# Kernel optimization log

Hardware: AMD Instinct MI355X
Metric: run time of the kernel (lower is better)

## Reference

```python
import jax, jax.numpy as jnp
import numpy as np

H = 1024  # hidden size

def _gru_layer(x, h0_l, w_ih_l, w_hh_l, b_ih_l, b_hh_l):
    # x: [T,B,I]; precompute input gates for all timesteps (like addmm in the kernel)
    x_gates = jnp.einsum('tbi,gi->tbg', x, w_ih_l) + b_ih_l  # [T,B,3H]

    def step(h, xg):
        # h: [B,H]; xg: [B,3H]
        h_gates = h @ w_hh_l.T + b_hh_l  # [B,3H]
        xr, xz, xn = xg[:, :H], xg[:, H:2*H], xg[:, 2*H:]
        hr, hz, hn = h_gates[:, :H], h_gates[:, H:2*H], h_gates[:, 2*H:]
        r = jax.nn.sigmoid(xr + hr)
        z = jax.nn.sigmoid(xz + hz)
        n = jnp.tanh(xn + r * hn)
        h_new = (1.0 - z) * n + z * h
        return h_new, h_new

    h_final, seq_out = jax.lax.scan(step, h0_l, x_gates)
    return h_final, seq_out


def setup_inputs() -> dict:
    key = jax.random.key(0)
    ks = jax.random.split(key, 6)
    T, B, I, L = 512, 64, 1024, 2
    s = 1.0 / np.sqrt(H)
    return {
        'x': jax.random.normal(ks[0], (T, B, I), dtype=jnp.float32),
        'h0': jax.random.normal(ks[1], (L, B, H), dtype=jnp.float32),
        'w_ih': jax.random.normal(ks[2], (L, 3 * H, I), dtype=jnp.float32) * s,
        'w_hh': jax.random.normal(ks[3], (L, 3 * H, H), dtype=jnp.float32) * s,
        'b_ih': jax.random.normal(ks[4], (L, 3 * H), dtype=jnp.float32) * s,
        'b_hh': jax.random.normal(ks[5], (L, 3 * H), dtype=jnp.float32) * s,
    }


def reference(x, h0, w_ih, w_hh, b_ih, b_hh):
    num_layers = h0.shape[0]
    h_n = []
    cur = x
    for l in range(num_layers):
        h_final, seq_out = _gru_layer(cur, h0[l], w_ih[l], w_hh[l], b_ih[l], b_hh[l])
        h_n.append(h_final)
        cur = seq_out  # layer output becomes next layer's input
    # kernel returns only the final hidden state of every layer, in fp32
    return jnp.stack(h_n, axis=0)  # [L,B,H]
```

## Files before the change

### kernel.cpp

```cpp
#include <hip/hip_runtime.h>

typedef unsigned short u16;
typedef unsigned long long u64;
typedef __attribute__((ext_vector_type(8))) short short8;
typedef __attribute__((ext_vector_type(4))) float f32x4;

#define HH 1024
#define BB 64
#define TT 512
#define G3 3072
#define NBLK 192
#define NS 513
#define SLOT (BB * HH)
#define FSTRIDE 32
#define RING 32

__device__ __forceinline__ u16 f2b(float f) {
  unsigned u = __float_as_uint(f);
  unsigned r = (u + 0x7fffu + ((u >> 16) & 1u)) >> 16;
  return (u16)r;
}
__device__ __forceinline__ float b2f(u16 h) {
  return __uint_as_float(((unsigned)h) << 16);
}
__device__ __forceinline__ float ftanh(float x) {
  x = fminf(15.f, fmaxf(-15.f, x));
  float e = __expf(2.f * x);
  return (e - 1.f) / (e + 1.f);
}

__device__ __forceinline__ void st_u32_agent(unsigned* p, unsigned v) {
  __hip_atomic_store(p, v, __ATOMIC_RELAXED, __HIP_MEMORY_SCOPE_AGENT);
}
__device__ __forceinline__ unsigned ld_u32_agent(const unsigned* p) {
  return __hip_atomic_load(p, __ATOMIC_RELAXED, __HIP_MEMORY_SCOPE_AGENT);
}


__global__ void f32_to_bf16_k(const float* __restrict__ s, u16* __restrict__ d, int n) {
  int stride = gridDim.x * blockDim.x * 4;
  for (int i = (blockIdx.x * blockDim.x + threadIdx.x) * 4; i < n; i += stride) {
    float4 v = *(const float4*)(s + i);
    uint2 p;
    p.x = (unsigned)f2b(v.x) | ((unsigned)f2b(v.y) << 16);
    p.y = (unsigned)f2b(v.z) | ((unsigned)f2b(v.w) << 16);
    *(uint2*)(d + i) = p;
  }
}

__global__ void init_h_k(const float* __restrict__ h0in, u16* __restrict__ hbuf0,
                         u16* __restrict__ hbuf1) {
  int i = blockIdx.x * blockDim.x + threadIdx.x;
  if (i < BB * HH) {
    hbuf0[i] = f2b(h0in[i]);
    hbuf1[i] = f2b(h0in[BB * HH + i]);
  }
}


__global__ __launch_bounds__(256) void gemm_xg_k(
    const u16* __restrict__ A, const u16* __restrict__ Wt,
    const float* __restrict__ bias, u16* __restrict__ C) {
  const int bm = blockIdx.x / 24;
  const int bn = blockIdx.x % 24;
  const int m0 = bm * 128, n0 = bn * 128;
  __shared__ __align__(16) u16 al[128 * 40];
  __shared__ __align__(16) u16 bl[128 * 40];
  const int tid = threadIdx.x;
  const int w = tid >> 6, l = tid & 63;
  const int wr = w >> 1, wc = w & 1;
  const int c0 = tid, c1 = tid + 256;
  const int r0 = c0 >> 2, s0 = c0 & 3, r1 = c1 >> 2, s1 = c1 & 3;

  const f32x4 fzero = {0.f, 0.f, 0.f, 0.f};
  f32x4 acc[4][4];
#pragma unroll
  for (int i = 0; i < 4; ++i)
#pragma unroll
    for (int j = 0; j < 4; ++j) acc[i][j] = fzero;

  const u16* a0p = A + (size_t)(m0 + r0) * 1024 + s0 * 8;
  const u16* a1p = A + (size_t)(m0 + r1) * 1024 + s1 * 8;
  const u16* b0p = Wt + (size_t)(n0 + r0) * 1024 + s0 * 8;
  const u16* b1p = Wt + (size_t)(n0 + r1) * 1024 + s1 * 8;

  int4 va0 = *(const int4*)(a0p);
  int4 va1 = *(const int4*)(a1p);
  int4 vb0 = *(const int4*)(b0p);
  int4 vb1 = *(const int4*)(b1p);

  for (int kt = 0; kt < 32; ++kt) {
    __syncthreads();
    *(int4*)&al[r0 * 40 + s0 * 8] = va0;
    *(int4*)&al[r1 * 40 + s1 * 8] = va1;
    *(int4*)&bl[r0 * 40 + s0 * 8] = vb0;
    *(int4*)&bl[r1 * 40 + s1 * 8] = vb1;
    __syncthreads();
    if (kt < 31) {
      va0 = *(const int4*)(a0p + (kt + 1) * 32);
      va1 = *(const int4*)(a1p + (kt + 1) * 32);
      vb0 = *(const int4*)(b0p + (kt + 1) * 32);
      vb1 = *(const int4*)(b1p + (kt + 1) * 32);
    }
    short8 af[4], bf[4];
#pragma unroll
    for (int i = 0; i < 4; ++i)
      af[i] = *(const short8*)&al[(wr * 64 + i * 16 + (l & 15)) * 40 + (l >> 4) * 8];
#pragma unroll
    for (int j = 0; j < 4; ++j)
      bf[j] = *(const short8*)&bl[(wc * 64 + j * 16 + (l & 15)) * 40 + (l >> 4) * 8];
#pragma unroll
    for (int i = 0; i < 4; ++i)
#pragma unroll
      for (int j = 0; j < 4; ++j)
        acc[i][j] = __builtin_amdgcn_mfma_f32_16x16x32_bf16(af[i], bf[j], acc[i][j], 0, 0, 0);
  }

#pragma unroll
  for (int i = 0; i < 4; ++i) {
#pragma unroll
    for (int j = 0; j < 4; ++j) {
      int col = n0 + wc * 64 + j * 16 + (l & 15);
      float bv = bias[col];
#pragma unroll
      for (int q = 0; q < 4; ++q) {
        int row = m0 + wr * 64 + i * 16 + (l >> 4) * 4 + q;
        C[(size_t)row * G3 + col] = f2b(acc[i][j][q] + bv);
      }
    }
  }
}


__global__ __launch_bounds__(256, 1) void gru_scan13_k(
    const u16* __restrict__ xg0,
    const u16* __restrict__ whh0, const u16* __restrict__ wih1,
    const u16* __restrict__ whh1,
    const float* __restrict__ bhh0, const float* __restrict__ bih1,
    const float* __restrict__ bhh1,
    const float* __restrict__ h0in,
    u16* __restrict__ hbuf0, u16* __restrict__ hbuf1,
    u16* __restrict__ xg1ring, float* __restrict__ out,
    unsigned* __restrict__ flags0, unsigned* __restrict__ flags1,
    unsigned* __restrict__ flags2) {
  const int blk = blockIdx.x;
  const int grp = blk >> 6;
  const int sub = blk & 63;
  const int tid = threadIdx.x;
  const int w = tid >> 6, l = tid & 63;
  const int lrow = l & 15;
  const int kb = (l >> 4) * 8;
  const int myrow0 = w * 16 + (l >> 4) * 4;
  const size_t arow = (size_t)(w * 16 + lrow) * HH + kb;
  const f32x4 fzero = {0.f, 0.f, 0.f, 0.f};

  __shared__ __align__(16) u16 wlds[48 * 1024];
  {
    const u16* Wsrc = (grp == 0) ? whh0 : (grp == 1) ? wih1 : whh1;
    for (int i = tid; i < 6144; i += 256) {
      int r = i >> 7;
      int c = i & 127;
      int g = r >> 4;
      int wrow = g * HH + sub * 16 + (r & 15);
      int4 v = *(const int4*)(Wsrc + (size_t)wrow * 1024 + c * 8);
      int idx = r * 1024 + ((c * 8) ^ ((r & 7) << 3));
      *(int4*)&wlds[idx] = v;
    }
  }
  __syncthreads();
  __builtin_amdgcn_fence(__ATOMIC_ACQUIRE, "agent");

  const int j = sub * 16 + lrow;
  const int sx = (lrow & 7) << 3;
  const int myf = (sub * 4 + w) * FSTRIDE;
  const int plf = (l * 4 + w) * FSTRIDE;

  if (grp == 0) {
    const float bhr = bhh0[j], bhz = bhh0[HH + j], bhn = bhh0[2 * HH + j];
    float hreg[4];
#pragma unroll
    for (int q = 0; q < 4; ++q) hreg[q] = h0in[(myrow0 + q) * HH + j];

    for (int t = 0; t < TT; ++t) {
      u16 xrv[4], xzv[4], xnv[4];
      const u16* xp = xg0 + (size_t)t * BB * G3;
#pragma unroll
      for (int q = 0; q < 4; ++q) {
        const u16* rp = xp + (size_t)(myrow0 + q) * G3;
        xrv[q] = rp[j]; xzv[q] = rp[HH + j]; xnv[q] = rp[2 * HH + j];
      }
      if (t > 0) {
        for (;;) {
          unsigned a0 = ld_u32_agent(&flags0[plf]);
          if (__all(a0 >= (unsigned)t)) break;
        }
      }
      __builtin_amdgcn_fence(__ATOMIC_ACQUIRE, "workgroup");

      const u16* Ap = hbuf0 + (size_t)t * SLOT + arow;
      short8 ar[32];
#pragma unroll
      for (int ks = 0; ks < 32; ++ks) ar[ks] = *(const short8*)(Ap + ks * 32);

      f32x4 acc0 = fzero, acc1 = fzero, acc2 = fzero;
#pragma unroll
      for (int ks = 0; ks < 32; ++ks) {
        int ke = kb + ks * 32;
        short8 b0 = *(const short8*)&wlds[(lrow) * 1024 + (ke ^ sx)];
        short8 b1 = *(const short8*)&wlds[(16 + lrow) * 1024 + (ke ^ sx)];
        short8 b2 = *(const short8*)&wlds[(32 + lrow) * 1024 + (ke ^ sx)];
        acc0 = __builtin_amdgcn_mfma_f32_16x16x32_bf16(ar[ks], b0, acc0, 0, 0, 0);
        acc1 = __builtin_amdgcn_mfma_f32_16x16x32_bf16(ar[ks], b1, acc1, 0, 0, 0);
        acc2 = __builtin_amdgcn_mfma_f32_16x16x32_bf16(ar[ks], b2, acc2, 0, 0, 0);
      }

      u16* hbn = hbuf0 + (size_t)(t + 1) * SLOT;
#pragma unroll
      for (int q = 0; q < 4; ++q) {
        float rr = acc0[q] + bhr + b2f(xrv[q]);
        float zz = acc1[q] + bhz + b2f(xzv[q]);
        float nn = acc2[q] + bhn;
        float r = 1.f / (1.f + __expf(-rr));
        float z = 1.f / (1.f + __expf(-zz));
        float n = ftanh(b2f(xnv[q]) + r * nn);
        float hv = (1.f - z) * n + z * hreg[q];
        hreg[q] = hv;
        int hb = (int)f2b(hv);
        int nb = __shfl_xor(hb, 1);
        if ((l & 1) == 0) {
          unsigned pk = (unsigned)(u16)hb | (((unsigned)(u16)nb) << 16);
          st_u32_agent((unsigned*)(hbn + (size_t)(myrow0 + q) * HH + j), pk);
        }
      }
      asm volatile("s_waitcnt vmcnt(0)" ::: "memory");
      if (l == 0) st_u32_agent(&flags0[myf], (unsigned)(t + 1));
    }
#pragma unroll
    for (int q = 0; q < 4; ++q) out[(size_t)(myrow0 + q) * HH + j] = hreg[q];

  } else if (grp == 1) {
    const float bir = bih1[j], biz = bih1[HH + j], bin = bih1[2 * HH + j];

    for (int t = 1; t <= TT; ++t) {
      for (;;) {
        unsigned a0 = ld_u32_agent(&flags0[plf]);
        unsigned f2 = ld_u32_agent(&flags2[myf]);
        int ok = (a0 >= (unsigned)t) && ((int)f2 >= t - RING);
        if (__all(ok)) break;
      }
      __builtin_amdgcn_fence(__ATOMIC_ACQUIRE, "workgroup");

      const u16* Ap = hbuf0 + (size_t)t * SLOT + arow;
      short8 ar[32];
#pragma unroll
      for (int ks = 0; ks < 32; ++ks) ar[ks] = *(const short8*)(Ap + ks * 32);

      f32x4 acc0 = fzero, acc1 = fzero, acc2 = fzero;
#pragma unroll
      for (int ks = 0; ks < 32; ++ks) {
        int ke = kb + ks * 32;
        short8 b0 = *(const short8*)&wlds[(lrow) * 1024 + (ke ^ sx)];
        short8 b1 = *(const short8*)&wlds[(16 + lrow) * 1024 + (ke ^ sx)];
        short8 b2 = *(const short8*)&wlds[(32 + lrow) * 1024 + (ke ^ sx)];
        acc0 = __builtin_amdgcn_mfma_f32_16x16x32_bf16(ar[ks], b0, acc0, 0, 0, 0);
        acc1 = __builtin_amdgcn_mfma_f32_16x16x32_bf16(ar[ks], b1, acc1, 0, 0, 0);
        acc2 = __builtin_amdgcn_mfma_f32_16x16x32_bf16(ar[ks], b2, acc2, 0, 0, 0);
      }

      u16* ox = xg1ring + (size_t)(t & (RING - 1)) * (BB * G3);
#pragma unroll
      for (int q = 0; q < 4; ++q) {
        int row = myrow0 + q;
        int a0v = (int)f2b(acc0[q] + bir); int a0n = __shfl_xor(a0v, 1);
        int a1v = (int)f2b(acc1[q] + biz); int a1n = __shfl_xor(a1v, 1);
        int a2v = (int)f2b(acc2[q] + bin); int a2n = __shfl_xor(a2v, 1);
        if ((l & 1) == 0) {
          st_u32_agent((unsigned*)(ox + (size_t)row * G3 + j),
                       (unsigned)(u16)a0v | (((unsigned)(u16)a0n) << 16));
          st_u32_agent((unsigned*)(ox + (size_t)row * G3 + HH + j),
                       (unsigned)(u16)a1v | (((unsigned)(u16)a1n) << 16));
          st_u32_agent((unsigned*)(ox + (size_t)row * G3 + 2 * HH + j),
                       (unsigned)(u16)a2v | (((unsigned)(u16)a2n) << 16));
        }
      }
      asm volatile("s_waitcnt vmcnt(0)" ::: "memory");
      if (l == 0) st_u32_agent(&flags1[myf], (unsigned)t);
    }

  } else {
    const float bhr = bhh1[j], bhz = bhh1[HH + j], bhn = bhh1[2 * HH + j];
    float hreg[4];
#pragma unroll
    for (int q = 0; q < 4; ++q) hreg[q] = h0in[BB * HH + (myrow0 + q) * HH + j];
    const int jpair = j & ~1;
    const int sel = (j & 1) * 16;

    for (int t = 1; t <= TT; ++t) {
      for (;;) {
        unsigned f1 = ld_u32_agent(&flags1[myf]);
        unsigned a2 = ld_u32_agent(&flags2[plf]);
        int ok = (f1 >= (unsigned)t) && (a2 >= (unsigned)(t - 1));
        if (__all(ok)) break;
      }
      __builtin_amdgcn_fence(__ATOMIC_ACQUIRE, "workgroup");

      const u16* ox = xg1ring + (size_t)(t & (RING - 1)) * (BB * G3);
      unsigned pr[4], pz[4], pn[4];
#pragma unroll
      for (int q = 0; q < 4; ++q) {
        const u16* rp = ox + (size_t)(myrow0 + q) * G3;
        pr[q] = ld_u32_agent((const unsigned*)(rp + jpair));
        pz[q] = ld_u32_agent((const unsigned*)(rp + HH + jpair));
        pn[q] = ld_u32_agent((const unsigned*)(rp + 2 * HH + jpair));
      }
      const u16* Ap = hbuf1 + (size_t)(t - 1) * SLOT + arow;
      short8 ar[32];
#pragma unroll
      for (int ks = 0; ks < 32; ++ks) ar[ks] = *(const short8*)(Ap + ks * 32);

      f32x4 acc0 = fzero, acc1 = fzero, acc2 = fzero;
#pragma unroll
      for (int ks = 0; ks < 32; ++ks) {
        int ke = kb + ks * 32;
        short8 b0 = *(const short8*)&wlds[(lrow) * 1024 + (ke ^ sx)];
        short8 b1 = *(const short8*)&wlds[(16 + lrow) * 1024 + (ke ^ sx)];
        short8 b2 = *(const short8*)&wlds[(32 + lrow) * 1024 + (ke ^ sx)];
        acc0 = __builtin_amdgcn_mfma_f32_16x16x32_bf16(ar[ks], b0, acc0, 0, 0, 0);
        acc1 = __builtin_amdgcn_mfma_f32_16x16x32_bf16(ar[ks], b1, acc1, 0, 0, 0);
        acc2 = __builtin_amdgcn_mfma_f32_16x16x32_bf16(ar[ks], b2, acc2, 0, 0, 0);
      }

      u16* hbn = hbuf1 + (size_t)t * SLOT;
#pragma unroll
      for (int q = 0; q < 4; ++q) {
        float rr = acc0[q] + bhr + b2f((u16)(pr[q] >> sel));
        float zz = acc1[q] + bhz + b2f((u16)(pz[q] >> sel));
        float nn = acc2[q] + bhn;
        float r = 1.f / (1.f + __expf(-rr));
        float z = 1.f / (1.f + __expf(-zz));
        float n = ftanh(b2f((u16)(pn[q] >> sel)) + r * nn);
        float hv = (1.f - z) * n + z * hreg[q];
        hreg[q] = hv;
        int hb = (int)f2b(hv);
        int nb = __shfl_xor(hb, 1);
        if ((l & 1) == 0) {
          unsigned pk = (unsigned)(u16)hb | (((unsigned)(u16)nb) << 16);
          st_u32_agent((unsigned*)(hbn + (size_t)(myrow0 + q) * HH + j), pk);
        }
      }
      asm volatile("s_waitcnt vmcnt(0)" ::: "memory");
      if (l == 0) st_u32_agent(&flags2[myf], (unsigned)t);
    }
#pragma unroll
    for (int q = 0; q < 4; ++q) out[BB * HH + (size_t)(myrow0 + q) * HH + j] = hreg[q];
  }
}


extern "C" void kernel_launch(void* const* d_in, const int* in_sizes, int n_in,
                              void* d_out, int out_size, void* d_ws, size_t ws_size,
                              hipStream_t stream) {
  const float* x   = (const float*)d_in[0];
  const float* h0  = (const float*)d_in[1];
  const float* wih = (const float*)d_in[2];
  const float* whh = (const float*)d_in[3];
  const float* bih = (const float*)d_in[4];
  const float* bhh = (const float*)d_in[5];
  float* out = (float*)d_out;

  char* ws = (char*)d_ws;
  size_t off = 0;
  auto alloc = [&](size_t bytes) -> void* {
    void* p = ws + off;
    off += (bytes + 255) & ~(size_t)255;
    return p;
  };
  u16* xg0   = (u16*)alloc((size_t)TT * BB * G3 * 2);
  u16* wihb  = (u16*)alloc((size_t)2 * G3 * HH * 2);
  u16* whhb  = (u16*)alloc((size_t)2 * G3 * HH * 2);
  size_t hbytes = (size_t)2 * NS * SLOT * 2;
  size_t xbytes = (size_t)TT * BB * HH * 2;
  char* un = (char*)alloc(hbytes > xbytes ? hbytes : xbytes);
  u16* xbf   = (u16*)un;
  u16* hbuf0 = (u16*)un;
  u16* hbuf1 = hbuf0 + (size_t)NS * SLOT;
  u16* xg1ring = (u16*)alloc((size_t)RING * BB * G3 * 2);
  unsigned* flags0 = (unsigned*)alloc(256 * FSTRIDE * 4);
  unsigned* flags1 = (unsigned*)alloc(256 * FSTRIDE * 4);
  unsigned* flags2 = (unsigned*)alloc(256 * FSTRIDE * 4);

  hipMemsetAsync(flags0, 0, 256 * FSTRIDE * 4, stream);
  hipMemsetAsync(flags1, 0, 256 * FSTRIDE * 4, stream);
  hipMemsetAsync(flags2, 0, 256 * FSTRIDE * 4, stream);
  f32_to_bf16_k<<<2048, 256, 0, stream>>>(x, xbf, TT * BB * HH);
  f32_to_bf16_k<<<512, 256, 0, stream>>>(wih, wihb, 2 * G3 * HH);
  f32_to_bf16_k<<<512, 256, 0, stream>>>(whh, whhb, 2 * G3 * HH);

  gemm_xg_k<<<6144, 256, 0, stream>>>(xbf, wihb, bih, xg0);

  init_h_k<<<256, 256, 0, stream>>>(h0, hbuf0, hbuf1);

  gru_scan13_k<<<NBLK, 256, 0, stream>>>(xg0,
                                         whhb, wihb + (size_t)G3 * HH, whhb + (size_t)G3 * HH,
                                         bhh, bih + G3, bhh + G3, h0,
                                         hbuf0, hbuf1, xg1ring, out,
                                         flags0, flags1, flags2);
}
```

Before: 5.391 ms.

## Stream recurrent GEMM over K chunks as producer blocks signal readiness

Replaces the all-or-nothing spin-wait before each step's recurrent GEMM with a single ballot over per-block ready flags. Each K chunk of the MFMA loop waits only for the two producer blocks that own those hidden columns, so compute can start while slower producers finish. Flags are coarsened from one per wave to one per block, published by thread 0 after a __syncthreads and a release fence. In exchange, the A-operand loads are no longer batched ahead of the MFMA loop and are issued inside a loop with data-dependent polling, which may expose global-load latency.

```diff
diff --git a/kernel.cpp b/kernel.cpp
--- a/kernel.cpp
+++ b/kernel.cpp
@@ -132,7 +132,30 @@
 }
 
 
-__global__ __launch_bounds__(256, 1) void gru_scan13_k(
+#define INORDER_GEMM(FLAGS, TGT, AP)                                          \
+  {                                                                           \
+    unsigned fv = ld_u32_agent(&FLAGS[l * FSTRIDE]);                          \
+    u64 ready = __ballot(fv >= (unsigned)(TGT));                              \
+    __builtin_amdgcn_fence(__ATOMIC_ACQUIRE, "workgroup");                    \
+    _Pragma("unroll")                                                         \
+    for (int ks = 0; ks < 32; ++ks) {                                         \
+      while (((ready >> (2 * ks)) & 3ull) != 3ull) {                          \
+        fv = ld_u32_agent(&FLAGS[l * FSTRIDE]);                               \
+        ready = __ballot(fv >= (unsigned)(TGT));                              \
+        __builtin_amdgcn_fence(__ATOMIC_ACQUIRE, "workgroup");                \
+      }                                                                       \
+      short8 a = *(const short8*)((AP) + ks * 32);                            \
+      int ke = kb + ks * 32;                                                  \
+      short8 b0 = *(const short8*)&wlds[(lrow) * 1024 + (ke ^ sx)];           \
+      short8 b1 = *(const short8*)&wlds[(16 + lrow) * 1024 + (ke ^ sx)];      \
+      short8 b2 = *(const short8*)&wlds[(32 + lrow) * 1024 + (ke ^ sx)];      \
+      acc0 = __builtin_amdgcn_mfma_f32_16x16x32_bf16(a, b0, acc0, 0, 0, 0);   \
+      acc1 = __builtin_amdgcn_mfma_f32_16x16x32_bf16(a, b1, acc1, 0, 0, 0);   \
+      acc2 = __builtin_amdgcn_mfma_f32_16x16x32_bf16(a, b2, acc2, 0, 0, 0);   \
+    }                                                                         \
+  }
+
+__global__ __launch_bounds__(256, 1) void gru_scan15_k(
     const u16* __restrict__ xg0,
     const u16* __restrict__ whh0, const u16* __restrict__ wih1,
     const u16* __restrict__ whh1,
@@ -172,8 +195,6 @@
 
   const int j = sub * 16 + lrow;
   const int sx = (lrow & 7) << 3;
-  const int myf = (sub * 4 + w) * FSTRIDE;
-  const int plf = (l * 4 + w) * FSTRIDE;
 
   if (grp == 0) {
     const float bhr = bhh0[j], bhz = bhh0[HH + j], bhn = bhh0[2 * HH + j];
@@ -189,29 +210,23 @@
         const u16* rp = xp + (size_t)(myrow0 + q) * G3;
         xrv[q] = rp[j]; xzv[q] = rp[HH + j]; xnv[q] = rp[2 * HH + j];
       }
-      if (t > 0) {
-        for (;;) {
-          unsigned a0 = ld_u32_agent(&flags0[plf]);
-          if (__all(a0 >= (unsigned)t)) break;
+
+      const u16* Ap = hbuf0 + (size_t)t * SLOT + arow;
+      f32x4 acc0 = fzero, acc1 = fzero, acc2 = fzero;
+      if (t == 0) {
+#pragma unroll
+        for (int ks = 0; ks < 32; ++ks) {
+          short8 a = *(const short8*)(Ap + ks * 32);
+          int ke = kb + ks * 32;
+          short8 b0 = *(const short8*)&wlds[(lrow) * 1024 + (ke ^ sx)];
+          short8 b1 = *(const short8*)&wlds[(16 + lrow) * 1024 + (ke ^ sx)];
+          short8 b2 = *(const short8*)&wlds[(32 + lrow) * 1024 + (ke ^ sx)];
+          acc0 = __builtin_amdgcn_mfma_f32_16x16x32_bf16(a, b0, acc0, 0, 0, 0);
+          acc1 = __builtin_amdgcn_mfma_f32_16x16x32_bf16(a, b1, acc1, 0, 0, 0);
+          acc2 = __builtin_amdgcn_mfma_f32_16x16x32_bf16(a, b2, acc2, 0, 0, 0);
         }
-      }
-      __builtin_amdgcn_fence(__ATOMIC_ACQUIRE, "workgroup");
-
-      const u16* Ap = hbuf0 + (size_t)t * SLOT + arow;
-      short8 ar[32];
-#pragma unroll
-      for (int ks = 0; ks < 32; ++ks) ar[ks] = *(const short8*)(Ap + ks * 32);
-
-      f32x4 acc0 = fzero, acc1 = fzero, acc2 = fzero;
-#pragma unroll
-      for (int ks = 0; ks < 32; ++ks) {
-        int ke = kb + ks * 32;
-        short8 b0 = *(const short8*)&wlds[(lrow) * 1024 + (ke ^ sx)];
-        short8 b1 = *(const short8*)&wlds[(16 + lrow) * 1024 + (ke ^ sx)];
-        short8 b2 = *(const short8*)&wlds[(32 + lrow) * 1024 + (ke ^ sx)];
-        acc0 = __builtin_amdgcn_mfma_f32_16x16x32_bf16(ar[ks], b0, acc0, 0, 0, 0);
-        acc1 = __builtin_amdgcn_mfma_f32_16x16x32_bf16(ar[ks], b1, acc1, 0, 0, 0);
-        acc2 = __builtin_amdgcn_mfma_f32_16x16x32_bf16(ar[ks], b2, acc2, 0, 0, 0);
+      } else {
+        INORDER_GEMM(flags0, t, Ap)
       }
 
       u16* hbn = hbuf0 + (size_t)(t + 1) * SLOT;
@@ -232,8 +247,12 @@
           st_u32_agent((unsigned*)(hbn + (size_t)(myrow0 + q) * HH + j), pk);
         }
       }
-      asm volatile("s_waitcnt vmcnt(0)" ::: "memory");
-      if (l == 0) st_u32_agent(&flags0[myf], (unsigned)(t + 1));
+
+      __syncthreads();
+      if (tid == 0) {
+        __builtin_amdgcn_fence(__ATOMIC_RELEASE, "workgroup");
+        st_u32_agent(&flags0[sub * FSTRIDE], (unsigned)(t + 1));
+      }
     }
 #pragma unroll
     for (int q = 0; q < 4; ++q) out[(size_t)(myrow0 + q) * HH + j] = hreg[q];
@@ -243,29 +262,13 @@
 
     for (int t = 1; t <= TT; ++t) {
       for (;;) {
-        unsigned a0 = ld_u32_agent(&flags0[plf]);
-        unsigned f2 = ld_u32_agent(&flags2[myf]);
-        int ok = (a0 >= (unsigned)t) && ((int)f2 >= t - RING);
-        if (__all(ok)) break;
-      }
-      __builtin_amdgcn_fence(__ATOMIC_ACQUIRE, "workgroup");
+        unsigned f2 = ld_u32_agent(&flags2[sub * FSTRIDE]);
+        if ((int)f2 >= t - RING) break;
+      }
 
       const u16* Ap = hbuf0 + (size_t)t * SLOT + arow;
-      short8 ar[32];
-#pragma unroll
-      for (int ks = 0; ks < 32; ++ks) ar[ks] = *(const short8*)(Ap + ks * 32);
-
       f32x4 acc0 = fzero, acc1 = fzero, acc2 = fzero;
-#pragma unroll
-      for (int ks = 0; ks < 32; ++ks) {
-        int ke = kb + ks * 32;
-        short8 b0 = *(const short8*)&wlds[(lrow) * 1024 + (ke ^ sx)];
-        short8 b1 = *(const short8*)&wlds[(16 + lrow) * 1024 + (ke ^ sx)];
-        short8 b2 = *(const short8*)&wlds[(32 + lrow) * 1024 + (ke ^ sx)];
-        acc0 = __builtin_amdgcn_mfma_f32_16x16x32_bf16(ar[ks], b0, acc0, 0, 0, 0);
-        acc1 = __builtin_amdgcn_mfma_f32_16x16x32_bf16(ar[ks], b1, acc1, 0, 0, 0);
-        acc2 = __builtin_amdgcn_mfma_f32_16x16x32_bf16(ar[ks], b2, acc2, 0, 0, 0);
-      }
+      INORDER_GEMM(flags0, t, Ap)
 
       u16* ox = xg1ring + (size_t)(t & (RING - 1)) * (BB * G3);
 #pragma unroll
@@ -283,8 +286,12 @@
                        (unsigned)(u16)a2v | (((unsigned)(u16)a2n) << 16));
         }
       }
-      asm volatile("s_waitcnt vmcnt(0)" ::: "memory");
-      if (l == 0) st_u32_agent(&flags1[myf], (unsigned)t);
+
+      __syncthreads();
+      if (tid == 0) {
+        __builtin_amdgcn_fence(__ATOMIC_RELEASE, "workgroup");
+        st_u32_agent(&flags1[sub * FSTRIDE], (unsigned)t);
+      }
     }
 
   } else {
@@ -297,10 +304,8 @@
 
     for (int t = 1; t <= TT; ++t) {
       for (;;) {
-        unsigned f1 = ld_u32_agent(&flags1[myf]);
-        unsigned a2 = ld_u32_agent(&flags2[plf]);
-        int ok = (f1 >= (unsigned)t) && (a2 >= (unsigned)(t - 1));
-        if (__all(ok)) break;
+        unsigned f1 = ld_u32_agent(&flags1[sub * FSTRIDE]);
+        if (f1 >= (unsigned)t) break;
       }
       __builtin_amdgcn_fence(__ATOMIC_ACQUIRE, "workgroup");
 
@@ -313,22 +318,10 @@
         pz[q] = ld_u32_agent((const unsigned*)(rp + HH + jpair));
         pn[q] = ld_u32_agent((const unsigned*)(rp + 2 * HH + jpair));
       }
+
       const u16* Ap = hbuf1 + (size_t)(t - 1) * SLOT + arow;
-      short8 ar[32];
-#pragma unroll
-      for (int ks = 0; ks < 32; ++ks) ar[ks] = *(const short8*)(Ap + ks * 32);
-
       f32x4 acc0 = fzero, acc1 = fzero, acc2 = fzero;
-#pragma unroll
-      for (int ks = 0; ks < 32; ++ks) {
-        int ke = kb + ks * 32;
-        short8 b0 = *(const short8*)&wlds[(lrow) * 1024 + (ke ^ sx)];
-        short8 b1 = *(const short8*)&wlds[(16 + lrow) * 1024 + (ke ^ sx)];
-        short8 b2 = *(const short8*)&wlds[(32 + lrow) * 1024 + (ke ^ sx)];
-        acc0 = __builtin_amdgcn_mfma_f32_16x16x32_bf16(ar[ks], b0, acc0, 0, 0, 0);
-        acc1 = __builtin_amdgcn_mfma_f32_16x16x32_bf16(ar[ks], b1, acc1, 0, 0, 0);
-        acc2 = __builtin_amdgcn_mfma_f32_16x16x32_bf16(ar[ks], b2, acc2, 0, 0, 0);
-      }
+      INORDER_GEMM(flags2, t - 1, Ap)
 
       u16* hbn = hbuf1 + (size_t)t * SLOT;
 #pragma unroll
@@ -348,8 +341,12 @@
           st_u32_agent((unsigned*)(hbn + (size_t)(myrow0 + q) * HH + j), pk);
         }
       }
-      asm volatile("s_waitcnt vmcnt(0)" ::: "memory");
-      if (l == 0) st_u32_agent(&flags2[myf], (unsigned)t);
+
+      __syncthreads();
+      if (tid == 0) {
+        __builtin_amdgcn_fence(__ATOMIC_RELEASE, "workgroup");
+        st_u32_agent(&flags2[sub * FSTRIDE], (unsigned)t);
+      }
     }
 #pragma unroll
     for (int q = 0; q < 4; ++q) out[BB * HH + (size_t)(myrow0 + q) * HH + j] = hreg[q];
@@ -385,13 +382,13 @@
   u16* hbuf0 = (u16*)un;
   u16* hbuf1 = hbuf0 + (size_t)NS * SLOT;
   u16* xg1ring = (u16*)alloc((size_t)RING * BB * G3 * 2);
-  unsigned* flags0 = (unsigned*)alloc(256 * FSTRIDE * 4);
-  unsigned* flags1 = (unsigned*)alloc(256 * FSTRIDE * 4);
-  unsigned* flags2 = (unsigned*)alloc(256 * FSTRIDE * 4);
-
-  hipMemsetAsync(flags0, 0, 256 * FSTRIDE * 4, stream);
-  hipMemsetAsync(flags1, 0, 256 * FSTRIDE * 4, stream);
-  hipMemsetAsync(flags2, 0, 256 * FSTRIDE * 4, stream);
+  unsigned* flags0 = (unsigned*)alloc(64 * FSTRIDE * 4);
+  unsigned* flags1 = (unsigned*)alloc(64 * FSTRIDE * 4);
+  unsigned* flags2 = (unsigned*)alloc(64 * FSTRIDE * 4);
+
+  hipMemsetAsync(flags0, 0, 64 * FSTRIDE * 4, stream);
+  hipMemsetAsync(flags1, 0, 64 * FSTRIDE * 4, stream);
+  hipMemsetAsync(flags2, 0, 64 * FSTRIDE * 4, stream);
   f32_to_bf16_k<<<2048, 256, 0, stream>>>(x, xbf, TT * BB * HH);
   f32_to_bf16_k<<<512, 256, 0, stream>>>(wih, wihb, 2 * G3 * HH);
   f32_to_bf16_k<<<512, 256, 0, stream>>>(whh, whhb, 2 * G3 * HH);
@@ -400,7 +397,7 @@
 
   init_h_k<<<256, 256, 0, stream>>>(h0, hbuf0, hbuf1);
 
-  gru_scan13_k<<<NBLK, 256, 0, stream>>>(xg0,
+  gru_scan15_k<<<NBLK, 256, 0, stream>>>(xg0,
                                          whhb, wihb + (size_t)G3 * HH, whhb + (size_t)G3 * HH,
                                          bhh, bih + G3, bhh + G3, h0,
                                          hbuf0, hbuf1, xg1ring, out,
```

Result: faster. 5.138 ms (-4.7%).
